# Kernel tuning notes

Hardware: AMD Instinct MI355X
Metric: run time of the kernel (lower is better)

Reference implementation:

```python
import jax, jax.numpy as jnp
import numpy as np

X_MIN, X_MAX = -51.2, 51.2
Y_MIN, Y_MAX = -51.2, 51.2
RES = 0.2
BEV_W = int((X_MAX - X_MIN) / RES)  # 512
BEV_H = int((Y_MAX - Y_MIN) / RES)  # 512
NUM_CELLS = BEV_W * BEV_H           # 262144
CLS_WEIGHT = 1.0
BOX_WEIGHT = 1.0


def setup_inputs() -> dict:
    key = jax.random.key(0)
    k1, k2, k3, k4, k5 = jax.random.split(key, 5)
    B, N, C, D = 8, 128, 10, 7
    cls_logits = jax.random.normal(k1, (B, NUM_CELLS, C), dtype=jnp.float32)
    box_preds = jax.random.normal(k2, (B, NUM_CELLS, D), dtype=jnp.float32)
    # gt boxes: x,y uniform in [-50, 50] (inside BEV), rest ~ N(0,1)-ish
    gt_boxes = jax.random.normal(k3, (B, N, D), dtype=jnp.float32)
    xy = jax.random.uniform(k3, (B, N, 2), minval=-50.0, maxval=50.0)
    gt_boxes = gt_boxes.at[..., :2].set(xy)
    gt_labels = jax.random.randint(k4, (B, N), 0, C, dtype=jnp.int64)
    gt_masks = jax.random.uniform(k5, (B, N), dtype=jnp.float32)
    return {"cls_logits": cls_logits, "box_preds": box_preds,
            "gt_boxes": gt_boxes, "gt_labels": gt_labels, "gt_masks": gt_masks}


def reference(cls_logits, box_preds, gt_boxes, gt_labels, gt_masks):
    B = cls_logits.shape[0]
    N = gt_boxes.shape[1]
    x = gt_boxes[..., 0]  # [B, N]
    y = gt_boxes[..., 1]
    valid = ((gt_masks > 0.5) & (gt_labels >= 0)
             & (x >= X_MIN) & (x <= X_MAX)
             & (y >= Y_MIN) & (y <= Y_MAX))
    gx = jnp.clip(((x - X_MIN) / RES).astype(jnp.int32), 0, BEV_W - 1)
    gy = jnp.clip(((y - Y_MIN) / RES).astype(jnp.int32), 0, BEV_H - 1)
    idx = gy * BEV_W + gx                       # [B, N]
    idx = jnp.where(valid, idx, NUM_CELLS)      # out-of-range -> dropped
    b_idx = jnp.broadcast_to(jnp.arange(B)[:, None], (B, N))
    lbl = jnp.clip(gt_labels, 0).astype(jnp.int32)

    cls_targets = jnp.zeros_like(cls_logits).at[b_idx, idx, lbl].set(1.0, mode='drop')
    box_targets = jnp.zeros_like(box_preds).at[b_idx, idx].set(gt_boxes, mode='drop')
    reg_masks = jnp.zeros((B, NUM_CELLS), cls_logits.dtype).at[b_idx, idx].set(1.0, mode='drop')

    # BCE with logits (stable)
    z, t = cls_logits, cls_targets
    bce = jnp.maximum(z, 0.0) - z * t + jnp.log1p(jnp.exp(-jnp.abs(z)))
    cls_loss = bce.sum(-1).mean()

    # Smooth L1 (beta = 1)
    d = box_preds - box_targets
    ad = jnp.abs(d)
    sl1 = jnp.where(ad < 1.0, 0.5 * d * d, ad - 0.5).sum(-1)  # [B, NUM_CELLS]
    box_loss = (sl1 * reg_masks).sum() / (reg_masks.sum() + 1e-6)

    total = CLS_WEIGHT * cls_loss + BOX_WEIGHT * box_loss
    return jnp.stack([total, cls_loss, box_loss])
```

## Files before the change

### kernel.cpp

```cpp
#include <hip/hip_runtime.h>
#include <math.h>

#define X_MIN_F   (-51.2f)
#define X_MAX_F   ( 51.2f)
#define RES_F     ( 0.2f)
#define BEV_W     512
#define BEV_H     512
#define NUM_CELLS (BEV_W * BEV_H)
#define C_CLS     10
#define D_BOX     7
#define BATCH     8
#define NPTS      128


__global__ __launch_bounds__(NPTS)
void bev_scatter_kernel(const float* __restrict__ cls_logits,
                        const float* __restrict__ box_preds,
                        const float* __restrict__ gt_boxes,
                        const int*   __restrict__ gt_labels,
                        const float* __restrict__ gt_masks,
                        double* __restrict__ ws)
{
    const int b = blockIdx.x;
    const int n = threadIdx.x;

    __shared__ int s_idx[NPTS];
    __shared__ int s_lbl[NPTS];

    const float* gb = gt_boxes + ((size_t)b * NPTS + n) * D_BOX;
    const float x = gb[0];
    const float y = gb[1];
    const float m = gt_masks[b * NPTS + n];
    const int   lраw_dummy = 0; (void)lраw_dummy;
    const int   lraw = gt_labels[b * NPTS + n];

    const bool valid = (m > 0.5f) && (lraw >= 0) &&
                       (x >= X_MIN_F) && (x <= X_MAX_F) &&
                       (y >= X_MIN_F) && (y <= X_MAX_F);

    int gx = (int)((x - X_MIN_F) / RES_F);
    int gy = (int)((y - X_MIN_F) / RES_F);
    gx = min(max(gx, 0), BEV_W - 1);
    gy = min(max(gy, 0), BEV_H - 1);
    const int idx = gy * BEV_W + gx;
    const int lbl = (lraw < 0) ? 0 : lraw;

    s_idx[n] = valid ? idx : -1;
    s_lbl[n] = lbl;
    __syncthreads();

    if (s_idx[n] >= 0) {
        bool firstReg = true, firstCls = true, lastBox = true;
        const int my_idx = s_idx[n];
        const int my_lbl = s_lbl[n];
        #pragma unroll 8
        for (int k = 0; k < NPTS; ++k) {
            if (k == n || s_idx[k] != my_idx) continue;
            if (k < n) {
                firstReg = false;
                if (s_lbl[k] == my_lbl) firstCls = false;
            } else {
                lastBox = false;
            }
        }

        if (firstCls) {
            const float z = cls_logits[((size_t)b * NUM_CELLS + my_idx) * C_CLS + my_lbl];
            atomicAdd(&ws[1], (double)z);
        }
        if (firstReg) {
            atomicAdd(&ws[3], 1.0);
        }
        if (lastBox) {
            const float* bp = box_preds + ((size_t)b * NUM_CELLS + my_idx) * D_BOX;
            float s = 0.0f;
            #pragma unroll
            for (int d = 0; d < D_BOX; ++d) {
                const float diff = bp[d] - gb[d];
                const float ad = fabsf(diff);
                s += (ad < 1.0f) ? 0.5f * diff * diff : (ad - 0.5f);
            }
            atomicAdd(&ws[2], (double)s);
        }
    }
}

__global__ __launch_bounds__(256)
void bce_sum_kernel(const float* __restrict__ z, unsigned int n_total,
                    double* __restrict__ ws)
{
    const unsigned int n4 = n_total >> 2;
    const float4* __restrict__ z4 = (const float4*)z;

    float acc = 0.0f;
    unsigned int i = blockIdx.x * blockDim.x + threadIdx.x;
    const unsigned int stride = gridDim.x * blockDim.x;
    for (; i < n4; i += stride) {
        const float4 v = z4[i];
        acc += fmaxf(v.x, 0.0f) + log1pf(expf(-fabsf(v.x)));
        acc += fmaxf(v.y, 0.0f) + log1pf(expf(-fabsf(v.y)));
        acc += fmaxf(v.z, 0.0f) + log1pf(expf(-fabsf(v.z)));
        acc += fmaxf(v.w, 0.0f) + log1pf(expf(-fabsf(v.w)));
    }

    #pragma unroll
    for (int off = 32; off > 0; off >>= 1)
        acc += __shfl_down(acc, off);

    __shared__ float wsum[4];
    const int lane = threadIdx.x & 63;
    const int wid  = threadIdx.x >> 6;
    if (lane == 0) wsum[wid] = acc;
    __syncthreads();
    if (threadIdx.x == 0) {
        const float blk = wsum[0] + wsum[1] + wsum[2] + wsum[3];
        atomicAdd(&ws[0], (double)blk);
    }
}

__global__ void finalize_kernel(const double* __restrict__ ws,
                                float* __restrict__ out)
{
    const double cls = (ws[0] - ws[1]) / (double)((size_t)BATCH * NUM_CELLS);
    const double box = ws[2] / (ws[3] + 1e-6);
    out[0] = (float)(cls + box);
    out[1] = (float)cls;
    out[2] = (float)box;
}

extern "C" void kernel_launch(void* const* d_in, const int* in_sizes, int n_in,
                              void* d_out, int out_size, void* d_ws, size_t ws_size,
                              hipStream_t stream)
{
    const float* cls_logits = (const float*)d_in[0];
    const float* box_preds  = (const float*)d_in[1];
    const float* gt_boxes   = (const float*)d_in[2];
    const int*   gt_labels  = (const int*)  d_in[3];
    const float* gt_masks   = (const float*)d_in[4];
    float*  out = (float*)d_out;
    double* ws  = (double*)d_ws;

    hipMemsetAsync(d_ws, 0, 4 * sizeof(double), stream);

    bev_scatter_kernel<<<BATCH, NPTS, 0, stream>>>(
        cls_logits, box_preds, gt_boxes, gt_labels, gt_masks, ws);

    const unsigned int n_total = (unsigned int)in_sizes[0];
    bce_sum_kernel<<<2048, 256, 0, stream>>>(cls_logits, n_total, ws);

    finalize_kernel<<<1, 1, 0, stream>>>(ws, out);
}
```

Measured before the change: 209.9 us.

## Use hardware exp2/log2 softplus, drop atomics, fuse scatter into finalize

Swaps the accurate expf/log1pf in the BCE reduction for the hardware v_exp_f32/v_log_f32 instructions, which cuts the transcendental ALU cost of the main streaming pass. The double atomics are replaced by per-block float partials, and the finalize kernel is now a 1024-thread block that also does the GT scatter/dedup work and reduces the partials. This removes the memset, one kernel launch and the atomic contention. The cost is lower precision in softplus, since log2(1+e) loses accuracy for small e compared with log1pf.

```diff
diff --git a/kernel.cpp b/kernel.cpp
--- a/kernel.cpp
+++ b/kernel.cpp
@@ -11,28 +11,93 @@
 #define D_BOX     7
 #define BATCH     8
 #define NPTS      128
+#define NPART     2048
 
+#define LOG2E_F   1.4426950408889634f
+#define LN2_F     0.6931471805599453f
 
-__global__ __launch_bounds__(NPTS)
-void bev_scatter_kernel(const float* __restrict__ cls_logits,
-                        const float* __restrict__ box_preds,
-                        const float* __restrict__ gt_boxes,
-                        const int*   __restrict__ gt_labels,
-                        const float* __restrict__ gt_masks,
-                        double* __restrict__ ws)
+#if defined(__has_builtin)
+#if __has_builtin(__builtin_amdgcn_exp2f)
+#define FAST_EXP2(x) __builtin_amdgcn_exp2f(x)
+#endif
+#if __has_builtin(__builtin_amdgcn_logf)
+#define FAST_LOG2(x) __builtin_amdgcn_logf(x)
+#endif
+#endif
+#ifndef FAST_EXP2
+__device__ __forceinline__ float __fast_exp2_asm(float x) {
+    float r; asm volatile("v_exp_f32 %0, %1" : "=v"(r) : "v"(x)); return r;
+}
+#define FAST_EXP2(x) __fast_exp2_asm(x)
+#endif
+#ifndef FAST_LOG2
+__device__ __forceinline__ float __fast_log2_asm(float x) {
+    float r; asm volatile("v_log_f32 %0, %1" : "=v"(r) : "v"(x)); return r;
+}
+#define FAST_LOG2(x) __fast_log2_asm(x)
+#endif
+
+__device__ __forceinline__ float softplus_hw(float z) {
+    const float e = FAST_EXP2(-LOG2E_F * fabsf(z));
+    return fmaxf(z, 0.0f) + LN2_F * FAST_LOG2(1.0f + e);
+}
+
+__global__ __launch_bounds__(256)
+void bce_partials_kernel(const float* __restrict__ z, unsigned int n_total,
+                         float* __restrict__ partials)
 {
-    const int b = blockIdx.x;
-    const int n = threadIdx.x;
+    const unsigned int n4 = n_total >> 2;
+    const float4* __restrict__ z4 = (const float4*)z;
 
-    __shared__ int s_idx[NPTS];
-    __shared__ int s_lbl[NPTS];
+    float a0 = 0.0f, a1 = 0.0f, a2 = 0.0f, a3 = 0.0f;
+    unsigned int i = blockIdx.x * blockDim.x + threadIdx.x;
+    const unsigned int stride = gridDim.x * blockDim.x;
+    for (; i < n4; i += stride) {
+        const float4 v = z4[i];
+        a0 += softplus_hw(v.x);
+        a1 += softplus_hw(v.y);
+        a2 += softplus_hw(v.z);
+        a3 += softplus_hw(v.w);
+    }
+    float acc = (a0 + a1) + (a2 + a3);
 
-    const float* gb = gt_boxes + ((size_t)b * NPTS + n) * D_BOX;
+    #pragma unroll
+    for (int off = 32; off > 0; off >>= 1)
+        acc += __shfl_down(acc, off);
+
+    __shared__ float wsum[4];
+    const int lane = threadIdx.x & 63;
+    const int wid  = threadIdx.x >> 6;
+    if (lane == 0) wsum[wid] = acc;
+    __syncthreads();
+    if (threadIdx.x == 0)
+        partials[blockIdx.x] = wsum[0] + wsum[1] + wsum[2] + wsum[3];
+}
+
+__global__ __launch_bounds__(1024)
+void finalize_kernel(const float* __restrict__ cls_logits,
+                     const float* __restrict__ box_preds,
+                     const float* __restrict__ gt_boxes,
+                     const int*   __restrict__ gt_labels,
+                     const float* __restrict__ gt_masks,
+                     const float* __restrict__ partials,
+                     float* __restrict__ out)
+{
+    const int t = threadIdx.x;
+    const int b = t >> 7;
+    const int lane = t & 63;
+    const int wid  = t >> 6;
+
+    __shared__ int    s_idx[BATCH * NPTS];
+    __shared__ int    s_lbl[BATCH * NPTS];
+    __shared__ float  s_c[16], s_b[16], s_r[16];
+    __shared__ double s_p[16];
+
+    const float* gb = gt_boxes + (size_t)t * D_BOX;
     const float x = gb[0];
     const float y = gb[1];
-    const float m = gt_masks[b * NPTS + n];
-    const int   lраw_dummy = 0; (void)lраw_dummy;
-    const int   lraw = gt_labels[b * NPTS + n];
+    const float m = gt_masks[t];
+    const int   lraw = gt_labels[t];
 
     const bool valid = (m > 0.5f) && (lraw >= 0) &&
                        (x >= X_MIN_F) && (x <= X_MAX_F) &&
@@ -45,34 +110,30 @@
     const int idx = gy * BEV_W + gx;
     const int lbl = (lraw < 0) ? 0 : lraw;
 
-    s_idx[n] = valid ? idx : -1;
-    s_lbl[n] = lbl;
+    s_idx[t] = valid ? idx : -1;
+    s_lbl[t] = lbl;
     __syncthreads();
 
-    if (s_idx[n] >= 0) {
+    float corr = 0.0f, boxs = 0.0f, regc = 0.0f;
+    if (s_idx[t] >= 0) {
         bool firstReg = true, firstCls = true, lastBox = true;
-        const int my_idx = s_idx[n];
-        const int my_lbl = s_lbl[n];
+        const int base = b << 7;
         #pragma unroll 8
-        for (int k = 0; k < NPTS; ++k) {
-            if (k == n || s_idx[k] != my_idx) continue;
-            if (k < n) {
+        for (int k = base; k < base + NPTS; ++k) {
+            if (k == t || s_idx[k] != idx) continue;
+            if (k < t) {
                 firstReg = false;
-                if (s_lbl[k] == my_lbl) firstCls = false;
+                if (s_lbl[k] == lbl) firstCls = false;
             } else {
                 lastBox = false;
             }
         }
-
-        if (firstCls) {
-            const float z = cls_logits[((size_t)b * NUM_CELLS + my_idx) * C_CLS + my_lbl];
-            atomicAdd(&ws[1], (double)z);
-        }
-        if (firstReg) {
-            atomicAdd(&ws[3], 1.0);
-        }
+        if (firstCls)
+            corr = cls_logits[((size_t)b * NUM_CELLS + idx) * C_CLS + lbl];
+        if (firstReg)
+            regc = 1.0f;
         if (lastBox) {
-            const float* bp = box_preds + ((size_t)b * NUM_CELLS + my_idx) * D_BOX;
+            const float* bp = box_preds + ((size_t)b * NUM_CELLS + idx) * D_BOX;
             float s = 0.0f;
             #pragma unroll
             for (int d = 0; d < D_BOX; ++d) {
@@ -80,52 +141,39 @@
                 const float ad = fabsf(diff);
                 s += (ad < 1.0f) ? 0.5f * diff * diff : (ad - 0.5f);
             }
-            atomicAdd(&ws[2], (double)s);
+            boxs = s;
         }
     }
-}
+    #pragma unroll
+    for (int off = 32; off > 0; off >>= 1) {
+        corr += __shfl_down(corr, off);
+        boxs += __shfl_down(boxs, off);
+        regc += __shfl_down(regc, off);
+    }
+    if (lane == 0) { s_c[wid] = corr; s_b[wid] = boxs; s_r[wid] = regc; }
 
-__global__ __launch_bounds__(256)
-void bce_sum_kernel(const float* __restrict__ z, unsigned int n_total,
-                    double* __restrict__ ws)
-{
-    const unsigned int n4 = n_total >> 2;
-    const float4* __restrict__ z4 = (const float4*)z;
-
-    float acc = 0.0f;
-    unsigned int i = blockIdx.x * blockDim.x + threadIdx.x;
-    const unsigned int stride = gridDim.x * blockDim.x;
-    for (; i < n4; i += stride) {
-        const float4 v = z4[i];
-        acc += fmaxf(v.x, 0.0f) + log1pf(expf(-fabsf(v.x)));
-        acc += fmaxf(v.y, 0.0f) + log1pf(expf(-fabsf(v.y)));
-        acc += fmaxf(v.z, 0.0f) + log1pf(expf(-fabsf(v.z)));
-        acc += fmaxf(v.w, 0.0f) + log1pf(expf(-fabsf(v.w)));
-    }
-
+    double p = (double)partials[t] + (double)partials[t + 1024];
     #pragma unroll
     for (int off = 32; off > 0; off >>= 1)
-        acc += __shfl_down(acc, off);
+        p += __shfl_down(p, off);
+    if (lane == 0) s_p[wid] = p;
+    __syncthreads();
 
-    __shared__ float wsum[4];
-    const int lane = threadIdx.x & 63;
-    const int wid  = threadIdx.x >> 6;
-    if (lane == 0) wsum[wid] = acc;
-    __syncthreads();
-    if (threadIdx.x == 0) {
-        const float blk = wsum[0] + wsum[1] + wsum[2] + wsum[3];
-        atomicAdd(&ws[0], (double)blk);
+    if (t == 0) {
+        double sum_bce = 0.0, sum_corr = 0.0, sum_box = 0.0, sum_reg = 0.0;
+        #pragma unroll
+        for (int w = 0; w < 16; ++w) {
+            sum_bce  += s_p[w];
+            sum_corr += (double)s_c[w];
+            sum_box  += (double)s_b[w];
+            sum_reg  += (double)s_r[w];
+        }
+        const double cls = (sum_bce - sum_corr) / (double)((size_t)BATCH * NUM_CELLS);
+        const double box = sum_box / (sum_reg + 1e-6);
+        out[0] = (float)(cls + box);
+        out[1] = (float)cls;
+        out[2] = (float)box;
     }
-}
-
-__global__ void finalize_kernel(const double* __restrict__ ws,
-                                float* __restrict__ out)
-{
-    const double cls = (ws[0] - ws[1]) / (double)((size_t)BATCH * NUM_CELLS);
-    const double box = ws[2] / (ws[3] + 1e-6);
-    out[0] = (float)(cls + box);
-    out[1] = (float)cls;
-    out[2] = (float)box;
 }
 
 extern "C" void kernel_launch(void* const* d_in, const int* in_sizes, int n_in,
@@ -137,16 +185,13 @@
     const float* gt_boxes   = (const float*)d_in[2];
     const int*   gt_labels  = (const int*)  d_in[3];
     const float* gt_masks   = (const float*)d_in[4];
-    float*  out = (float*)d_out;
-    double* ws  = (double*)d_ws;
-
-    hipMemsetAsync(d_ws, 0, 4 * sizeof(double), stream);
-
-    bev_scatter_kernel<<<BATCH, NPTS, 0, stream>>>(
-        cls_logits, box_preds, gt_boxes, gt_labels, gt_masks, ws);
+    float* out      = (float*)d_out;
+    float* partials = (float*)d_ws;
 
     const unsigned int n_total = (unsigned int)in_sizes[0];
-    bce_sum_kernel<<<2048, 256, 0, stream>>>(cls_logits, n_total, ws);
 
-    finalize_kernel<<<1, 1, 0, stream>>>(ws, out);
+    bce_partials_kernel<<<NPART, 256, 0, stream>>>(cls_logits, n_total, partials);
+
+    finalize_kernel<<<1, 1024, 0, stream>>>(
+        cls_logits, box_preds, gt_boxes, gt_labels, gt_masks, partials, out);
 }
```

Result: faster. 178.1 us (-15.1%).
